# Kernel tuning notes

Hardware: AMD Instinct MI355X
Metric: run time of the kernel (lower is better)

## Reference

```python
import jax, jax.numpy as jnp
import numpy as np

B, S, H = 4, 2048, 896
NH, NKV, HD = 14, 2, 64
ROPE_THETA = 1e6


def setup_inputs() -> dict:
    key = jax.random.key(0)
    ks = jax.random.split(key, 8)
    s = 0.02
    return {
        "hidden_states": jax.random.normal(ks[0], (B, S, H), jnp.float32),
        "position_ids": jnp.arange(S, dtype=jnp.int64 if jax.config.jax_enable_x64 else jnp.int32)[None, :],
        "Wq": jax.random.normal(ks[1], (NH * HD, H), jnp.float32) * s,
        "bq": jax.random.normal(ks[2], (NH * HD,), jnp.float32) * s,
        "Wk": jax.random.normal(ks[3], (NKV * HD, H), jnp.float32) * s,
        "bk": jax.random.normal(ks[4], (NKV * HD,), jnp.float32) * s,
        "Wv": jax.random.normal(ks[5], (NKV * HD, H), jnp.float32) * s,
        "bv": jax.random.normal(ks[6], (NKV * HD,), jnp.float32) * s,
        "Wo": jax.random.normal(ks[7], (H, NH * HD), jnp.float32) * s,
    }


def _rope_cos_sin(position_ids, dtype):
    # inv_freq: [HD/2]
    inv_freq = 1.0 / (ROPE_THETA ** (jnp.arange(0, HD, 2, dtype=jnp.float32) / HD))
    # freqs: [1, S, HD/2]
    freqs = position_ids.astype(jnp.float32)[:, :, None] * inv_freq[None, None, :]
    emb = jnp.concatenate([freqs, freqs], axis=-1)  # [1, S, HD]
    return jnp.cos(emb).astype(dtype), jnp.sin(emb).astype(dtype)


def _rotate_half(x):
    x1, x2 = x[..., : HD // 2], x[..., HD // 2 :]
    return jnp.concatenate([-x2, x1], axis=-1)


def reference(hidden_states, position_ids, Wq, bq, Wk, bk, Wv, bv, Wo):
    bsz, q_len, _ = hidden_states.shape
    q = hidden_states @ Wq.T + bq  # [B,S,NH*HD]
    k = hidden_states @ Wk.T + bk  # [B,S,NKV*HD]
    v = hidden_states @ Wv.T + bv
    q = q.reshape(bsz, q_len, NH, HD).transpose(0, 2, 1, 3)    # [B,NH,S,HD]
    k = k.reshape(bsz, q_len, NKV, HD).transpose(0, 2, 1, 3)   # [B,NKV,S,HD]
    v = v.reshape(bsz, q_len, NKV, HD).transpose(0, 2, 1, 3)

    cos, sin = _rope_cos_sin(position_ids, hidden_states.dtype)
    cos, sin = cos[:, None, :, :], sin[:, None, :, :]  # broadcast over heads
    q = q * cos + _rotate_half(q) * sin
    k = k * cos + _rotate_half(k) * sin

    # GQA: repeat kv heads to NH
    n_rep = NH // NKV
    k = jnp.repeat(k, n_rep, axis=1)  # [B,NH,S,HD]
    v = jnp.repeat(v, n_rep, axis=1)

    scale = 1.0 / jnp.sqrt(jnp.asarray(HD, hidden_states.dtype))
    scores = jnp.einsum("bhqd,bhkd->bhqk", q, k) * scale  # [B,NH,S,S]
    causal = jnp.tril(jnp.ones((q_len, q_len), dtype=bool))
    scores = jnp.where(causal[None, None], scores, jnp.finfo(scores.dtype).min)
    probs = jax.nn.softmax(scores, axis=-1)
    attn = jnp.einsum("bhqk,bhkd->bhqd", probs, v)  # [B,NH,S,HD]
    attn = attn.transpose(0, 2, 1, 3).reshape(bsz, q_len, NH * HD)
    return attn @ Wo.T
```

## Files before the change

kernel.cpp:

```cpp
#include <hip/hip_runtime.h>
#include <stdint.h>

#define SB    2048
#define HID   896
#define NHEADS 14
#define NKVH  2
#define HDIM  64
#define BATCH 4
#define MROWS (BATCH*SB)
#define KVW   (NKVH*HDIM)
#define PANEL (SB*HDIM)

typedef short bfrag __attribute__((ext_vector_type(8)));
typedef float f32x4 __attribute__((ext_vector_type(4)));

__device__ __forceinline__ float b2f(unsigned short u) {
    unsigned int x = ((unsigned int)u) << 16;
    float f;
    __builtin_memcpy(&f, &x, 4);
    return f;
}
__device__ __forceinline__ unsigned short f2b(float f) {
    unsigned int x;
    __builtin_memcpy(&x, &f, 4);
    x += 0x7fffu + ((x >> 16) & 1u);
    return (unsigned short)(x >> 16);
}
__device__ __forceinline__ unsigned int pack_bf16(float lo, float hi) {
    unsigned int a, b;
    __builtin_memcpy(&a, &lo, 4);
    __builtin_memcpy(&b, &hi, 4);
    return __builtin_amdgcn_perm(b, a, 0x07060302);
}

__device__ __forceinline__ void async16(void* lds, const void* g) {
    __builtin_amdgcn_global_load_lds(
        (const __attribute__((address_space(1))) unsigned int*)g,
        (__attribute__((address_space(3))) unsigned int*)lds, 16, 0, 0);
}

#define N_HS  (MROWS*HID)
#define N_WQ  (HID*HID)
#define N_BQ  (HID)
#define N_WK  (KVW*HID)
#define N_BK  (KVW)
#define N_WO  (HID*HID)
#define C0 ((size_t)N_HS)
#define C1 (C0 + N_WQ)
#define C2 (C1 + N_BQ)
#define C3 (C2 + N_WK)
#define C4 (C3 + N_BK)
#define C5 (C4 + N_WK)
#define C6 (C5 + N_BK)
#define C7 (C6 + N_WO)

__global__ __launch_bounds__(256) void cvt_kernel(
    const float* __restrict__ a0, const float* __restrict__ a1,
    const float* __restrict__ a2, const float* __restrict__ a3,
    const float* __restrict__ a4, const float* __restrict__ a5,
    const float* __restrict__ a6, const float* __restrict__ a7,
    unsigned short* __restrict__ d0, unsigned short* __restrict__ d1,
    unsigned short* __restrict__ d2, unsigned short* __restrict__ d3,
    unsigned short* __restrict__ d4, unsigned short* __restrict__ d5,
    unsigned short* __restrict__ d6, unsigned short* __restrict__ d7)
{
    size_t i = ((size_t)blockIdx.x * 256 + threadIdx.x) * 4;
    if (i >= C7) return;
    const float* s; unsigned short* d; size_t off;
    if      (i < C0) { s = a0; d = d0; off = i; }
    else if (i < C1) { s = a1; d = d1; off = i - C0; }
    else if (i < C2) { s = a2; d = d2; off = i - C1; }
    else if (i < C3) { s = a3; d = d3; off = i - C2; }
    else if (i < C4) { s = a4; d = d4; off = i - C3; }
    else if (i < C5) { s = a5; d = d5; off = i - C4; }
    else if (i < C6) { s = a6; d = d6; off = i - C5; }
    else             { s = a7; d = d7; off = i - C6; }
    float4 v = *(const float4*)(s + off);
    ushort4 o;
    o.x = f2b(v.x); o.y = f2b(v.y); o.z = f2b(v.z); o.w = f2b(v.w);
    *(ushort4*)(d + off) = o;
}

template<int EPI>
__device__ __forceinline__ void gemm128(
    unsigned short* __restrict__ Al, unsigned short* __restrict__ Bl,
    const unsigned short* __restrict__ A, int lda,
    const unsigned short* __restrict__ W, int ldw,
    const unsigned short* __restrict__ bias,
    void* __restrict__ Cv, int ldc, int m0, int n0, int K,
    unsigned short* __restrict__ VT)
{
    const int tid  = threadIdx.x;
    const int wave = tid >> 6;
    const int lane = tid & 63;
    const int col  = lane & 15;
    const int quad = lane >> 4;
    const int wm   = (wave >> 1) * 64;
    const int wn   = (wave & 1) * 64;
    const int srow = lane >> 2;
    const int scol = (lane & 3) * 8;

    f32x4 acc[4][4] = {};

    for (int k0 = 0; k0 < K; k0 += 32) {
#pragma unroll
        for (int i = 0; i < 2; ++i) {
            const int c = wave*2 + i;
            async16(Al + c*512, A + (size_t)(m0 + c*16 + srow)*lda + k0 + scol);
            async16(Bl + c*512, W + (size_t)(n0 + c*16 + srow)*ldw + k0 + scol);
        }
        __syncthreads();
        bfrag a[4], b[4];
#pragma unroll
        for (int mb = 0; mb < 4; ++mb)
            a[mb] = *(const bfrag*)(Al + (wm + mb*16 + col)*32 + quad*8);
#pragma unroll
        for (int nb = 0; nb < 4; ++nb)
            b[nb] = *(const bfrag*)(Bl + (wn + nb*16 + col)*32 + quad*8);
#pragma unroll
        for (int mb = 0; mb < 4; ++mb)
#pragma unroll
            for (int nb = 0; nb < 4; ++nb)
                acc[mb][nb] = __builtin_amdgcn_mfma_f32_16x16x32_bf16(
                    a[mb], b[nb], acc[mb][nb], 0, 0, 0);
        __syncthreads();
    }

    if (EPI == 2) {
#pragma unroll
        for (int nb = 0; nb < 4; ++nb) {
            const int n = wn + nb*16 + col;
            const float bv = b2f(bias[n]);
            const int kvh = n >> 6;
#pragma unroll
            for (int mb = 0; mb < 4; ++mb) {
                const int m = m0 + wm + mb*16 + quad*4;
                const int bb = m >> 11, s = m & (SB-1);
                const int cc = (s >> 5) & 1;
                const int qv = (s >> 3) & 3;
                const int jb = s & 7;
                ushort4 w;
                w.x = f2b(acc[mb][nb][0] + bv);
                w.y = f2b(acc[mb][nb][1] + bv);
                w.z = f2b(acc[mb][nb][2] + bv);
                w.w = f2b(acc[mb][nb][3] + bv);
                *(ushort4*)(VT + (size_t)(bb*NKVH + kvh)*PANEL
                            + (size_t)((s >> 6)*8 + cc*4 + nb)*512
                            + (qv*16 + col)*8 + jb) = w;
            }
        }
    } else {
#pragma unroll
        for (int nb = 0; nb < 4; ++nb) {
            const int n = n0 + wn + nb*16 + col;
            const float bv = bias ? b2f(bias[n]) : 0.0f;
#pragma unroll
            for (int mb = 0; mb < 4; ++mb) {
                const size_t base = (size_t)(m0 + wm + mb*16 + quad*4) * ldc + n;
#pragma unroll
                for (int r = 0; r < 4; ++r) {
                    const float v = acc[mb][nb][r] + bv;
                    if (EPI == 1) ((float*)Cv)[base + (size_t)r * ldc] = v;
                    else ((unsigned short*)Cv)[base + (size_t)r * ldc] = f2b(v);
                }
            }
        }
    }
}

__global__ __launch_bounds__(256) void qkv_gemm(
    const unsigned short* __restrict__ hs,
    const unsigned short* __restrict__ Wq, const unsigned short* __restrict__ bq,
    const unsigned short* __restrict__ Wk, const unsigned short* __restrict__ bk,
    const unsigned short* __restrict__ Wv, const unsigned short* __restrict__ bv,
    unsigned short* __restrict__ Qw, unsigned short* __restrict__ Kw,
    unsigned short* __restrict__ Vp)
{
    __shared__ __align__(16) unsigned short Al[128*32];
    __shared__ __align__(16) unsigned short Bl[128*32];
    const int m0  = blockIdx.x * 128;
    const int seg = blockIdx.y;
    if (seg < 7)
        gemm128<0>(Al, Bl, hs, HID, Wq, HID, bq, Qw, HID, m0, seg*128, HID, nullptr);
    else if (seg == 7)
        gemm128<0>(Al, Bl, hs, HID, Wk, HID, bk, Kw, KVW, m0, 0, HID, nullptr);
    else
        gemm128<2>(Al, Bl, hs, HID, Wv, HID, bv, nullptr, 0, m0, 0, HID, Vp);
}

__global__ __launch_bounds__(256) void out_gemm(
    const unsigned short* __restrict__ Aw, const unsigned short* __restrict__ Wo,
    float* __restrict__ out)
{
    __shared__ __align__(16) unsigned short Al[128*32];
    __shared__ __align__(16) unsigned short Bl[128*32];
    gemm128<1>(Al, Bl, Aw, HID, Wo, HID, nullptr, out, HID,
               blockIdx.x * 128, blockIdx.y * 128, HID, nullptr);
}

__global__ __launch_bounds__(256) void rope_kernel(unsigned short* __restrict__ Q,
                                                   const unsigned short* __restrict__ Kw,
                                                   unsigned short* __restrict__ Kp)
{
    const int idx  = blockIdx.x * 256 + threadIdx.x;
    const int pair = idx & 31;
    const int head = (idx >> 5) & 15;
    const int m    = idx >> 9;
    const int pos  = m & (SB - 1);
    const float inv = exp2f(-(float)(2*pair) * (19.9315685693f / 64.0f));
    const float f = (float)pos * inv;
    float s, c;
    sincosf(f, &s, &c);
    if (head < NHEADS) {
        const float mul = 0.1803368801111f;
        unsigned short* base = Q + (size_t)m * HID + (size_t)head * HDIM;
        const float x1 = b2f(base[pair]);
        const float x2 = b2f(base[pair + 32]);
        base[pair]      = f2b((x1 * c - x2 * s) * mul);
        base[pair + 32] = f2b((x2 * c + x1 * s) * mul);
    } else {
        const int kvh = head - NHEADS;
        const unsigned short* src = Kw + (size_t)m * KVW + (size_t)kvh * HDIM;
        const float x1 = b2f(src[pair]);
        const float x2 = b2f(src[pair + 32]);
        const float y1 = x1 * c - x2 * s;
        const float y2 = x2 * c + x1 * s;
        const int bb = m >> 11, sq = m & (SB - 1);
        const int tile = sq >> 6, r6 = sq & 63;
        const int kb = r6 >> 4, colk = r6 & 15;
        const int quad = pair >> 3, j = pair & 7;
        unsigned short* panel = Kp + (size_t)(bb*NKVH + kvh) * PANEL;
        const size_t off0 = (size_t)(tile*8 + kb*2)*512 + (quad*16 + colk)*8 + j;
        panel[off0]       = f2b(y1);
        panel[off0 + 512] = f2b(y2);
    }
}

__global__ __launch_bounds__(64, 2) void flash_kernel(
    const unsigned short* __restrict__ Q,
    const unsigned short* __restrict__ Kp,
    const unsigned short* __restrict__ Vp,
    unsigned short* __restrict__ Aw)
{
    const int bid  = blockIdx.x;
    const int cidx = bid / 56;
    const int hb   = bid - cidx * 56;
    const int h    = hb % NHEADS;
    const int b    = hb / NHEADS;
    const int kvh  = h / 7;
    const int chunk = 63 - cidx;

    const int lane = threadIdx.x;
    const int col  = lane & 15;
    const int quad = lane >> 4;

    const int idxA = (col + ((quad & 1) << 5)) << 2;
    const int idxB = idxA + 64;
    const bool hi  = (quad >= 2);

    const unsigned short* Qb  = Q  + (size_t)b * SB * HID + (size_t)h * HDIM;
    const unsigned short* Kpp = Kp + (size_t)(b*NKVH + kvh) * PANEL;
    const unsigned short* Vpp = Vp + (size_t)(b*NKVH + kvh) * PANEL;

    bfrag ones;
#pragma unroll
    for (int jj = 0; jj < 8; ++jj) ones[jj] = (short)0x3F80;

    const int qrow  = chunk * 32;
    const int nsteps = (chunk >> 1) + 1;

    bfrag qf[2][2];
#pragma unroll
    for (int qb = 0; qb < 2; ++qb) {
        const unsigned short* qr = Qb + (size_t)(qrow + qb*16 + col) * HID;
        qf[qb][0] = *(const bfrag*)(qr + quad*8);
        qf[qb][1] = *(const bfrag*)(qr + 32 + quad*8);
    }

    f32x4 o[2][4] = {};
    f32x4 lac[2] = {};

    bfrag kc[4][2], kn[4][2];
#pragma unroll
    for (int kb = 0; kb < 4; ++kb) {
        kc[kb][0] = *(const bfrag*)(Kpp + (size_t)(kb*2 + 0)*512 + lane*8);
        kc[kb][1] = *(const bfrag*)(Kpp + (size_t)(kb*2 + 1)*512 + lane*8);
    }

    for (int step = 0; step < nsteps; ++step) {
        const size_t T = (size_t)step * 4096;
        const bool more = (step + 1 < nsteps);
        if (more) {
#pragma unroll
            for (int kb = 0; kb < 4; ++kb) {
                kn[kb][0] = *(const bfrag*)(Kpp + T + 4096 + (kb*2+0)*512 + lane*8);
                kn[kb][1] = *(const bfrag*)(Kpp + T + 4096 + (kb*2+1)*512 + lane*8);
            }
        }
        bfrag vf[2][4];
#pragma unroll
        for (int cc = 0; cc < 2; ++cc)
#pragma unroll
            for (int nb = 0; nb < 4; ++nb)
                vf[cc][nb] = *(const bfrag*)(Vpp + T + (cc*4 + nb)*512 + lane*8);

        f32x4 s[2][4];
#pragma unroll
        for (int kb = 0; kb < 4; ++kb)
#pragma unroll
            for (int qb = 0; qb < 2; ++qb) {
                f32x4 z = {};
                z = __builtin_amdgcn_mfma_f32_16x16x32_bf16(kc[kb][0], qf[qb][0], z, 0, 0, 0);
                z = __builtin_amdgcn_mfma_f32_16x16x32_bf16(kc[kb][1], qf[qb][1], z, 0, 0, 0);
                s[qb][kb] = z;
            }

        const int k0 = step * 64;
        unsigned int pk[2][4][2];
#pragma unroll
        for (int qb = 0; qb < 2; ++qb) {
            float pv[4][4];
#pragma unroll
            for (int kb = 0; kb < 4; ++kb)
#pragma unroll
                for (int r = 0; r < 4; ++r)
                    pv[kb][r] = __builtin_amdgcn_exp2f(s[qb][kb][r]);
            if (step == nsteps - 1) {
                const int q = qrow + qb*16 + col;
#pragma unroll
                for (int kb = 0; kb < 4; ++kb)
#pragma unroll
                    for (int r = 0; r < 4; ++r)
                        if (k0 + kb*16 + quad*4 + r > q) pv[kb][r] = 0.f;
            }
#pragma unroll
            for (int kb = 0; kb < 4; ++kb) {
                pk[qb][kb][0] = pack_bf16(pv[kb][0], pv[kb][1]);
                pk[qb][kb][1] = pack_bf16(pv[kb][2], pv[kb][3]);
            }
        }

#pragma unroll
        for (int cc = 0; cc < 2; ++cc)
#pragma unroll
            for (int qb = 0; qb < 2; ++qb) {
                unsigned int D[4];
#pragma unroll
                for (int jj = 0; jj < 4; ++jj) {
                    const int idx = (jj < 2) ? idxA : idxB;
                    const int t0 = __builtin_amdgcn_ds_bpermute(idx, (int)pk[qb][2*cc][jj & 1]);
                    const int t1 = __builtin_amdgcn_ds_bpermute(idx, (int)pk[qb][2*cc+1][jj & 1]);
                    D[jj] = (unsigned int)(hi ? t1 : t0);
                }
                bfrag pf;
                __builtin_memcpy(&pf, D, 16);
                lac[qb] = __builtin_amdgcn_mfma_f32_16x16x32_bf16(ones, pf, lac[qb], 0, 0, 0);
#pragma unroll
                for (int nb = 0; nb < 4; ++nb)
                    o[qb][nb] = __builtin_amdgcn_mfma_f32_16x16x32_bf16(
                        vf[cc][nb], pf, o[qb][nb], 0, 0, 0);
            }

        if (more) {
#pragma unroll
            for (int kb = 0; kb < 4; ++kb) {
                kc[kb][0] = kn[kb][0];
                kc[kb][1] = kn[kb][1];
            }
        }
    }

#pragma unroll
    for (int qb = 0; qb < 2; ++qb) {
        const float inv = 1.0f / lac[qb][0];
        const size_t row = (size_t)b * SB + qrow + qb*16 + col;
#pragma unroll
        for (int nb = 0; nb < 4; ++nb) {
            ushort4 w;
            w.x = f2b(o[qb][nb][0] * inv);
            w.y = f2b(o[qb][nb][1] * inv);
            w.z = f2b(o[qb][nb][2] * inv);
            w.w = f2b(o[qb][nb][3] * inv);
            *(ushort4*)(Aw + row * HID + h*HDIM + nb*16 + quad*4) = w;
        }
    }
}

extern "C" void kernel_launch(void* const* d_in, const int* in_sizes, int n_in,
                              void* d_out, int out_size, void* d_ws, size_t ws_size,
                              hipStream_t stream)
{
    (void)in_sizes; (void)n_in; (void)out_size; (void)ws_size;
    const float* hs_f = (const float*)d_in[0];
    const float* Wq_f = (const float*)d_in[2];
    const float* bq_f = (const float*)d_in[3];
    const float* Wk_f = (const float*)d_in[4];
    const float* bk_f = (const float*)d_in[5];
    const float* Wv_f = (const float*)d_in[6];
    const float* bv_f = (const float*)d_in[7];
    const float* Wo_f = (const float*)d_in[8];
    float* out = (float*)d_out;

    char* ws = (char*)d_ws;
    auto take = [&](size_t elems) {
        unsigned short* p = (unsigned short*)ws;
        ws += ((elems * 2 + 255) & ~(size_t)255);
        return p;
    };
    unsigned short* hs = take(N_HS);
    unsigned short* Wq = take(N_WQ);
    unsigned short* bq = take(N_BQ);
    unsigned short* Wk = take(N_WK);
    unsigned short* bk = take(N_BK);
    unsigned short* Wv = take(N_WK);
    unsigned short* bv = take(N_BK);
    unsigned short* Wo = take(N_WO);
    unsigned short* Qw = take((size_t)MROWS * HID);
    unsigned short* Kw = take((size_t)MROWS * KVW);
    unsigned short* Kp = take((size_t)MROWS * KVW);
    unsigned short* Vp = take((size_t)MROWS * KVW);
    unsigned short* Aw = take((size_t)MROWS * HID);

    cvt_kernel<<<dim3((C7/4 + 255)/256), 256, 0, stream>>>(
        hs_f, Wq_f, bq_f, Wk_f, bk_f, Wv_f, bv_f, Wo_f,
        hs, Wq, bq, Wk, bk, Wv, bv, Wo);
    qkv_gemm<<<dim3(MROWS/128, 9), 256, 0, stream>>>(hs, Wq, bq, Wk, bk, Wv, bv,
                                                     Qw, Kw, Vp);
    rope_kernel<<<dim3((MROWS*16*32)/256), 256, 0, stream>>>(Qw, Kw, Kp);
    flash_kernel<<<dim3(64*NHEADS*BATCH), 64, 0, stream>>>(Qw, Kp, Vp, Aw);
    out_gemm<<<dim3(MROWS/128, HID/128), 256, 0, stream>>>(Aw, Wo, out);
}
```

Before: 217.5 us.

## Double-buffer GEMM LDS, software-pipeline flash QK scores, precompute RoPE table

The shared GEMM routine now double-buffers its LDS tiles, issuing the async loads for the next K slice before computing on the current one. This removes one barrier per iteration and overlaps global loads with MFMA work. The flash kernel computes the next step's QK scores while the current step's exp and PV work is in flight, which overlaps MFMA latency but holds more registers. RoPE cos/sin values are precomputed once into a table by a new kernel, so each element no longer runs its own sincos, at the cost of an extra launch and a table read.

```diff
diff --git a/kernel.cpp b/kernel.cpp
--- a/kernel.cpp
+++ b/kernel.cpp
@@ -102,21 +102,31 @@
 
     f32x4 acc[4][4] = {};
 
-    for (int k0 = 0; k0 < K; k0 += 32) {
+    auto stage = [&](int buf, int k0) {
 #pragma unroll
         for (int i = 0; i < 2; ++i) {
             const int c = wave*2 + i;
-            async16(Al + c*512, A + (size_t)(m0 + c*16 + srow)*lda + k0 + scol);
-            async16(Bl + c*512, W + (size_t)(n0 + c*16 + srow)*ldw + k0 + scol);
-        }
-        __syncthreads();
+            async16(Al + buf*4096 + c*512,
+                    A + (size_t)(m0 + c*16 + srow)*lda + k0 + scol);
+            async16(Bl + buf*4096 + c*512,
+                    W + (size_t)(n0 + c*16 + srow)*ldw + k0 + scol);
+        }
+    };
+
+    stage(0, 0);
+    __syncthreads();
+    int cur = 0;
+    for (int k0 = 0; k0 < K; k0 += 32) {
+        if (k0 + 32 < K) stage(cur ^ 1, k0 + 32);
+        const unsigned short* Ab = Al + cur*4096;
+        const unsigned short* Bb = Bl + cur*4096;
         bfrag a[4], b[4];
 #pragma unroll
         for (int mb = 0; mb < 4; ++mb)
-            a[mb] = *(const bfrag*)(Al + (wm + mb*16 + col)*32 + quad*8);
+            a[mb] = *(const bfrag*)(Ab + (wm + mb*16 + col)*32 + quad*8);
 #pragma unroll
         for (int nb = 0; nb < 4; ++nb)
-            b[nb] = *(const bfrag*)(Bl + (wn + nb*16 + col)*32 + quad*8);
+            b[nb] = *(const bfrag*)(Bb + (wn + nb*16 + col)*32 + quad*8);
 #pragma unroll
         for (int mb = 0; mb < 4; ++mb)
 #pragma unroll
@@ -124,6 +134,7 @@
                 acc[mb][nb] = __builtin_amdgcn_mfma_f32_16x16x32_bf16(
                     a[mb], b[nb], acc[mb][nb], 0, 0, 0);
         __syncthreads();
+        cur ^= 1;
     }
 
     if (EPI == 2) {
@@ -176,41 +187,50 @@
     unsigned short* __restrict__ Qw, unsigned short* __restrict__ Kw,
     unsigned short* __restrict__ Vp)
 {
-    __shared__ __align__(16) unsigned short Al[128*32];
-    __shared__ __align__(16) unsigned short Bl[128*32];
+    __shared__ __align__(16) unsigned short Al[2][128*32];
+    __shared__ __align__(16) unsigned short Bl[2][128*32];
     const int m0  = blockIdx.x * 128;
     const int seg = blockIdx.y;
     if (seg < 7)
-        gemm128<0>(Al, Bl, hs, HID, Wq, HID, bq, Qw, HID, m0, seg*128, HID, nullptr);
+        gemm128<0>(&Al[0][0], &Bl[0][0], hs, HID, Wq, HID, bq, Qw, HID, m0, seg*128, HID, nullptr);
     else if (seg == 7)
-        gemm128<0>(Al, Bl, hs, HID, Wk, HID, bk, Kw, KVW, m0, 0, HID, nullptr);
+        gemm128<0>(&Al[0][0], &Bl[0][0], hs, HID, Wk, HID, bk, Kw, KVW, m0, 0, HID, nullptr);
     else
-        gemm128<2>(Al, Bl, hs, HID, Wv, HID, bv, nullptr, 0, m0, 0, HID, Vp);
+        gemm128<2>(&Al[0][0], &Bl[0][0], hs, HID, Wv, HID, bv, nullptr, 0, m0, 0, HID, Vp);
 }
 
 __global__ __launch_bounds__(256) void out_gemm(
     const unsigned short* __restrict__ Aw, const unsigned short* __restrict__ Wo,
     float* __restrict__ out)
 {
-    __shared__ __align__(16) unsigned short Al[128*32];
-    __shared__ __align__(16) unsigned short Bl[128*32];
-    gemm128<1>(Al, Bl, Aw, HID, Wo, HID, nullptr, out, HID,
+    __shared__ __align__(16) unsigned short Al[2][128*32];
+    __shared__ __align__(16) unsigned short Bl[2][128*32];
+    gemm128<1>(&Al[0][0], &Bl[0][0], Aw, HID, Wo, HID, nullptr, out, HID,
                blockIdx.x * 128, blockIdx.y * 128, HID, nullptr);
+}
+
+__global__ __launch_bounds__(256) void trig_kernel(float2* __restrict__ tab)
+{
+    const int i = blockIdx.x * 256 + threadIdx.x;
+    const int pos = i >> 5, pair = i & 31;
+    const float inv = exp2f(-(float)(2*pair) * (19.9315685693f / 64.0f));
+    float s, c;
+    sincosf((float)pos * inv, &s, &c);
+    tab[i] = make_float2(c, s);
 }
 
 __global__ __launch_bounds__(256) void rope_kernel(unsigned short* __restrict__ Q,
                                                    const unsigned short* __restrict__ Kw,
-                                                   unsigned short* __restrict__ Kp)
+                                                   unsigned short* __restrict__ Kp,
+                                                   const float2* __restrict__ tab)
 {
     const int idx  = blockIdx.x * 256 + threadIdx.x;
     const int pair = idx & 31;
     const int head = (idx >> 5) & 15;
     const int m    = idx >> 9;
     const int pos  = m & (SB - 1);
-    const float inv = exp2f(-(float)(2*pair) * (19.9315685693f / 64.0f));
-    const float f = (float)pos * inv;
-    float s, c;
-    sincosf(f, &s, &c);
+    const float2 cs = tab[pos*32 + pair];
+    const float c = cs.x, s = cs.y;
     if (head < NHEADS) {
         const float mul = 0.1803368801111f;
         unsigned short* base = Q + (size_t)m * HID + (size_t)head * HDIM;
@@ -280,16 +300,30 @@
     f32x4 o[2][4] = {};
     f32x4 lac[2] = {};
 
-    bfrag kc[4][2], kn[4][2];
-#pragma unroll
-    for (int kb = 0; kb < 4; ++kb) {
-        kc[kb][0] = *(const bfrag*)(Kpp + (size_t)(kb*2 + 0)*512 + lane*8);
-        kc[kb][1] = *(const bfrag*)(Kpp + (size_t)(kb*2 + 1)*512 + lane*8);
+    f32x4 scur[2][4];
+    {
+        bfrag kc0[4][2];
+#pragma unroll
+        for (int kb = 0; kb < 4; ++kb) {
+            kc0[kb][0] = *(const bfrag*)(Kpp + (size_t)(kb*2 + 0)*512 + lane*8);
+            kc0[kb][1] = *(const bfrag*)(Kpp + (size_t)(kb*2 + 1)*512 + lane*8);
+        }
+#pragma unroll
+        for (int kb = 0; kb < 4; ++kb)
+#pragma unroll
+            for (int qb = 0; qb < 2; ++qb) {
+                f32x4 z = {};
+                z = __builtin_amdgcn_mfma_f32_16x16x32_bf16(kc0[kb][0], qf[qb][0], z, 0, 0, 0);
+                z = __builtin_amdgcn_mfma_f32_16x16x32_bf16(kc0[kb][1], qf[qb][1], z, 0, 0, 0);
+                scur[qb][kb] = z;
+            }
     }
 
     for (int step = 0; step < nsteps; ++step) {
         const size_t T = (size_t)step * 4096;
         const bool more = (step + 1 < nsteps);
+
+        bfrag kn[4][2];
         if (more) {
 #pragma unroll
             for (int kb = 0; kb < 4; ++kb) {
@@ -304,17 +338,6 @@
             for (int nb = 0; nb < 4; ++nb)
                 vf[cc][nb] = *(const bfrag*)(Vpp + T + (cc*4 + nb)*512 + lane*8);
 
-        f32x4 s[2][4];
-#pragma unroll
-        for (int kb = 0; kb < 4; ++kb)
-#pragma unroll
-            for (int qb = 0; qb < 2; ++qb) {
-                f32x4 z = {};
-                z = __builtin_amdgcn_mfma_f32_16x16x32_bf16(kc[kb][0], qf[qb][0], z, 0, 0, 0);
-                z = __builtin_amdgcn_mfma_f32_16x16x32_bf16(kc[kb][1], qf[qb][1], z, 0, 0, 0);
-                s[qb][kb] = z;
-            }
-
         const int k0 = step * 64;
         unsigned int pk[2][4][2];
 #pragma unroll
@@ -324,7 +347,7 @@
             for (int kb = 0; kb < 4; ++kb)
 #pragma unroll
                 for (int r = 0; r < 4; ++r)
-                    pv[kb][r] = __builtin_amdgcn_exp2f(s[qb][kb][r]);
+                    pv[kb][r] = __builtin_amdgcn_exp2f(scur[qb][kb][r]);
             if (step == nsteps - 1) {
                 const int q = qrow + qb*16 + col;
 #pragma unroll
@@ -338,6 +361,19 @@
                 pk[qb][kb][0] = pack_bf16(pv[kb][0], pv[kb][1]);
                 pk[qb][kb][1] = pack_bf16(pv[kb][2], pv[kb][3]);
             }
+        }
+
+        f32x4 snext[2][4];
+        if (more) {
+#pragma unroll
+            for (int kb = 0; kb < 4; ++kb)
+#pragma unroll
+                for (int qb = 0; qb < 2; ++qb) {
+                    f32x4 z = {};
+                    z = __builtin_amdgcn_mfma_f32_16x16x32_bf16(kn[kb][0], qf[qb][0], z, 0, 0, 0);
+                    z = __builtin_amdgcn_mfma_f32_16x16x32_bf16(kn[kb][1], qf[qb][1], z, 0, 0, 0);
+                    snext[qb][kb] = z;
+                }
         }
 
 #pragma unroll
@@ -363,10 +399,10 @@
 
         if (more) {
 #pragma unroll
-            for (int kb = 0; kb < 4; ++kb) {
-                kc[kb][0] = kn[kb][0];
-                kc[kb][1] = kn[kb][1];
-            }
+            for (int qb = 0; qb < 2; ++qb)
+#pragma unroll
+                for (int kb = 0; kb < 4; ++kb)
+                    scur[qb][kb] = snext[qb][kb];
         }
     }
 
@@ -402,6 +438,8 @@
     float* out = (float*)d_out;
 
     char* ws = (char*)d_ws;
+    float2* tab = (float2*)ws;
+    ws += ((size_t)SB * 32 * sizeof(float2) + 255) & ~(size_t)255;
     auto take = [&](size_t elems) {
         unsigned short* p = (unsigned short*)ws;
         ws += ((elems * 2 + 255) & ~(size_t)255);
@@ -421,12 +459,13 @@
     unsigned short* Vp = take((size_t)MROWS * KVW);
     unsigned short* Aw = take((size_t)MROWS * HID);
 
+    trig_kernel<<<dim3(SB*32/256), 256, 0, stream>>>(tab);
     cvt_kernel<<<dim3((C7/4 + 255)/256), 256, 0, stream>>>(
         hs_f, Wq_f, bq_f, Wk_f, bk_f, Wv_f, bv_f, Wo_f,
         hs, Wq, bq, Wk, bk, Wv, bv, Wo);
     qkv_gemm<<<dim3(MROWS/128, 9), 256, 0, stream>>>(hs, Wq, bq, Wk, bk, Wv, bv,
                                                      Qw, Kw, Vp);
-    rope_kernel<<<dim3((MROWS*16*32)/256), 256, 0, stream>>>(Qw, Kw, Kp);
+    rope_kernel<<<dim3((MROWS*16*32)/256), 256, 0, stream>>>(Qw, Kw, Kp, tab);
     flash_kernel<<<dim3(64*NHEADS*BATCH), 64, 0, stream>>>(Qw, Kp, Vp, Aw);
     out_gemm<<<dim3(MROWS/128, HID/128), 256, 0, stream>>>(Aw, Wo, out);
 }
```

New measurement: 202.0 us. 7.1% less time.
